# Kernel tuning notes

Measured on AMD Instinct MI355X. Metric: run time of the kernel, lower is better.

Reference implementation:

```python
import jax, jax.numpy as jnp
import numpy as np

N, E, G, H = 50000, 800000, 2048, 128
DIS = 3  # dis_emb is None -> raw frac_diff (3 dims)
EIN = 2 * H + 6 + DIS  # 265


def _lin_init(key, fan_in, fan_out):
    lim = 1.0 / np.sqrt(fan_in)
    return jax.random.uniform(key, (fan_in, fan_out), jnp.float32, -lim, lim)


def setup_inputs() -> dict:
    key = jax.random.key(0)
    ks = jax.random.split(key, 12)
    node_features = jax.random.normal(ks[0], (N, H), jnp.float32)
    frac_coords = jax.random.uniform(ks[1], (N, 3), jnp.float32)
    lattices = jax.random.normal(ks[2], (G, 6), jnp.float32)
    frac_diff = jax.random.normal(ks[3], (E, 3), jnp.float32)
    edge_index = jax.random.randint(ks[4], (2, E), 0, N, jnp.int64 if jax.config.jax_enable_x64 else jnp.int32)
    edge2graph = jax.random.randint(ks[5], (E,), 0, G, edge_index.dtype)
    return dict(
        node_features=node_features,
        frac_coords=frac_coords,
        lattices=lattices,
        frac_diff=frac_diff,
        edge_index=edge_index,
        edge2graph=edge2graph,
        e_w1=_lin_init(ks[6], EIN, H), e_b1=jnp.zeros((H,), jnp.float32),
        e_w2=_lin_init(ks[7], H, H), e_b2=jnp.zeros((H,), jnp.float32),
        n_w1=_lin_init(ks[8], 2 * H, H), n_b1=jnp.zeros((H,), jnp.float32),
        n_w2=_lin_init(ks[9], H, H), n_b2=jnp.zeros((H,), jnp.float32),
    )


def reference(node_features, frac_coords, lattices, frac_diff, edge_index, edge2graph,
              e_w1, e_b1, e_w2, e_b2, n_w1, n_b1, n_w2, n_b2):
    n_nodes = node_features.shape[0]
    silu = jax.nn.silu
    # edge model: gather endpoints, concat with per-graph lattice + frac_diff
    hi = node_features[edge_index[0]]            # [E, H]
    hj = node_features[edge_index[1]]            # [E, H]
    lat = lattices[edge2graph]                   # [E, 6]
    edges_input = jnp.concatenate([hi, hj, lat, frac_diff], axis=1)  # [E, 265]
    e = silu(edges_input @ e_w1 + e_b1)
    edge_features = silu(e @ e_w2 + e_b2)        # [E, H]
    # scatter-mean aggregate onto source nodes
    seg = edge_index[0]
    agg_sum = jax.ops.segment_sum(edge_features, seg, num_segments=n_nodes)
    cnt = jax.ops.segment_sum(jnp.ones((edge_features.shape[0],), edge_features.dtype), seg, num_segments=n_nodes)
    agg = agg_sum / jnp.maximum(cnt, 1.0)[:, None]
    # node model + residual
    h = jnp.concatenate([node_features, agg], axis=1)  # [N, 2H]
    h = silu(h @ n_w1 + n_b1)
    node_output = silu(h @ n_w2 + n_b2)
    return node_features + node_output
```

## Files before the change

### kernel.cpp

```cpp
#include <hip/hip_runtime.h>

#define N_NODES 50000
#define N_EDGES 800000
#define HDIM 128
#define N_GRAPH 2048

typedef __bf16 bf16x8 __attribute__((ext_vector_type(8)));
typedef float f32x4 __attribute__((ext_vector_type(4)));
typedef float f32x16 __attribute__((ext_vector_type(16)));

static __device__ __forceinline__ unsigned short f2bf(float f) {
    unsigned int u = __float_as_uint(f);
    u += 0x7fffu + ((u >> 16) & 1u);
    return (unsigned short)(u >> 16);
}
static __device__ __forceinline__ float bflo(unsigned int u) { return __uint_as_float(u << 16); }
static __device__ __forceinline__ float bfhi(unsigned int u) { return __uint_as_float(u & 0xFFFF0000u); }

static __device__ __forceinline__ unsigned int cvt_pk_bf16(float lo, float hi) {
    unsigned int r;
    asm("v_cvt_pk_bf16_f32 %0, %1, %2" : "=v"(r) : "v"(lo), "v"(hi));
    return r;
}

static __device__ __forceinline__ float silu_f(float x) {
    float e = __builtin_amdgcn_exp2f(x * -1.44269504f);
    return x * __builtin_amdgcn_rcpf(1.0f + e);
}

#define PREP_BLOCKS 1408
#define HIST_BLOCKS 3125
#define ZERO_BLOCKS 6250
__global__ void prep_hist_kernel(const float* __restrict__ ew1, const float* __restrict__ ew2,
                                 const float* __restrict__ nw1, const float* __restrict__ nw2,
                                 const float* __restrict__ eb1, const float* __restrict__ lattices,
                                 const int* __restrict__ eidx,
                                 unsigned short* __restrict__ W1aT, unsigned short* __restrict__ W1bT,
                                 unsigned short* __restrict__ W2t, unsigned short* __restrict__ N1t,
                                 unsigned short* __restrict__ N2t, unsigned short* __restrict__ Lb,
                                 int* __restrict__ buf, float* __restrict__ agg) {
    const int bid = blockIdx.x;
    if (bid >= PREP_BLOCKS + HIST_BLOCKS) {
        const int idx = (bid - PREP_BLOCKS - HIST_BLOCKS) * 256 + threadIdx.x;
        ((float4*)agg)[idx] = make_float4(0.f, 0.f, 0.f, 0.f);
        return;
    }
    if (bid >= PREP_BLOCKS) {
        int e = (bid - PREP_BLOCKS) * 256 + threadIdx.x;
        if (e < N_EDGES) atomicAdd(&buf[eidx[e]], 1);
        return;
    }
    int i = bid * 256 + threadIdx.x;
    if (i < 16384) {
        int n = i >> 7, k = i & 127;
        W1aT[i] = f2bf(ew1[k * 128 + n]);
    } else if (i < 32768) {
        int j = i - 16384; int n = j >> 7, k = j & 127;
        W1bT[j] = f2bf(ew1[(128 + k) * 128 + n]);
    } else if (i < 49152) {
        int j = i - 32768; int n = j >> 7, k = j & 127;
        W2t[j] = f2bf(ew2[k * 128 + n]);
    } else if (i < 81920) {
        int j = i - 49152; int n = j >> 8, k = j & 255;
        N1t[j] = f2bf(nw1[k * 128 + n]);
    } else if (i < 98304) {
        int j = i - 81920; int n = j >> 7, k = j & 127;
        N2t[j] = f2bf(nw2[k * 128 + n]);
    } else if (i < 98304 + 262144) {
        int j = i - 98304; int g = j >> 7, c = j & 127;
        float s = eb1[c];
#pragma unroll
        for (int t = 0; t < 6; ++t) s += lattices[g * 6 + t] * ew1[(256 + t) * 128 + c];
        Lb[j] = f2bf(s);
    }
}

__global__ __launch_bounds__(1024) void scan_kernel(int* __restrict__ buf) {
    constexpr int CH = 12288;
    __shared__ int lds[CH];
    __shared__ int part[1024];
    __shared__ int carry_s;
    const int t = threadIdx.x;
    if (t == 0) carry_s = 0;
    __syncthreads();
#pragma unroll 1
    for (int base = 0; base < N_NODES; base += CH) {
#pragma unroll
        for (int k = 0; k < CH / 1024; ++k) {
            int f = k * 1024 + t;
            lds[f] = (base + f < N_NODES) ? buf[base + f] : 0;
        }
        __syncthreads();
        int loc[12];
        int s = 0;
#pragma unroll
        for (int i = 0; i < 12; ++i) { loc[i] = lds[t * 12 + i]; s += loc[i]; }
        part[t] = s;
        __syncthreads();
        for (int off = 1; off < 1024; off <<= 1) {
            int tmp = (t >= off) ? part[t - off] : 0;
            __syncthreads();
            part[t] += tmp;
            __syncthreads();
        }
        const int total = part[1023];
        int run = carry_s + part[t] - s;
#pragma unroll
        for (int i = 0; i < 12; ++i) { int tmp = loc[i]; lds[t * 12 + i] = run; run += tmp; }
        __syncthreads();
#pragma unroll
        for (int k = 0; k < CH / 1024; ++k) {
            int f = k * 1024 + t;
            if (base + f < N_NODES) buf[base + f] = lds[f];
        }
        __syncthreads();
        if (t == 0) carry_s += total;
        __syncthreads();
    }
}

#define PERM_BLOCKS2 3125
#define PQ_BLOCKS ((N_NODES + 63) / 64)
__global__ __launch_bounds__(256, 4) void perm_pq_kernel(
    const int* __restrict__ eidx, const int* __restrict__ e2g,
    const float* __restrict__ frac_diff, int* __restrict__ buf,
    unsigned short* __restrict__ perm_lo, unsigned char* __restrict__ perm_hi,
    uint4* __restrict__ rec, const int packed,
    const float* __restrict__ nf, const unsigned short* __restrict__ W1aT,
    const unsigned short* __restrict__ W1bT,
    unsigned short* __restrict__ P, unsigned short* __restrict__ Qm) {
    constexpr int SA = 136;
    __shared__ unsigned short sm[64 * SA];
    const int bid = blockIdx.x;
    const int tid = threadIdx.x;

    if (bid < PERM_BLOCKS2) {
        int e = bid * 256 + tid;
        if (e < N_EDGES) {
            int s = eidx[e];
            int pos = atomicAdd(&buf[s], 1);
            if (packed) {
                int d = eidx[N_EDGES + e];
                int g = e2g[e];
                unsigned int w0 = (unsigned int)s | ((unsigned int)d << 16);
                unsigned int w1 = (unsigned int)g | ((unsigned int)f2bf(frac_diff[3 * e]) << 16);
                unsigned int w2 = (unsigned int)f2bf(frac_diff[3 * e + 1]) |
                                  ((unsigned int)f2bf(frac_diff[3 * e + 2]) << 16);
                rec[pos] = make_uint4(w0, w1, w2, 0u);
            } else {
                perm_lo[pos] = (unsigned short)(e & 0xFFFF);
                perm_hi[pos] = (unsigned char)(e >> 16);
            }
        }
        return;
    }

    const int n0 = (bid - PERM_BLOCKS2) * 64;
    const int mrow = tid >> 2, q = tid & 3;
    {
        const int node = n0 + mrow;
        unsigned short* row = sm + mrow * SA + q * 32;
        if (node < N_NODES) {
            const float4* a4 = (const float4*)(nf + (size_t)node * HDIM) + q * 8;
#pragma unroll
            for (int j = 0; j < 8; ++j) {
                float4 v = a4[j];
                *(ushort4*)(row + 4 * j) = make_ushort4(f2bf(v.x), f2bf(v.y), f2bf(v.z), f2bf(v.w));
            }
        } else {
#pragma unroll
            for (int j = 0; j < 8; ++j) *(ushort4*)(row + 4 * j) = make_ushort4(0, 0, 0, 0);
        }
    }
    __syncthreads();

    const int wave = tid >> 6, lane = tid & 63;
    const int lr = lane & 15, kq = lane >> 4;
    f32x4 acca[8] = {}, accb[8] = {};
    const int arow = (wave * 16 + lr) * SA;
#pragma unroll
    for (int ks = 0; ks < 128; ks += 32) {
        bf16x8 a = *(const bf16x8*)(sm + arow + ks + kq * 8);
#pragma unroll
        for (int nt = 0; nt < 8; ++nt) {
            bf16x8 ba = *(const bf16x8*)(W1aT + (nt * 16 + lr) * 128 + ks + kq * 8);
            acca[nt] = __builtin_amdgcn_mfma_f32_16x16x32_bf16(a, ba, acca[nt], 0, 0, 0);
            bf16x8 bb = *(const bf16x8*)(W1bT + (nt * 16 + lr) * 128 + ks + kq * 8);
            accb[nt] = __builtin_amdgcn_mfma_f32_16x16x32_bf16(a, bb, accb[nt], 0, 0, 0);
        }
    }
    __syncthreads();

    const int node = n0 + mrow;
#pragma unroll
    for (int nt = 0; nt < 8; ++nt) {
        const int col = nt * 16 + lr;
#pragma unroll
        for (int r = 0; r < 4; ++r)
            sm[(wave * 16 + kq * 4 + r) * SA + col] = f2bf(acca[nt][r]);
    }
    __syncthreads();
    if (node < N_NODES) {
        uint4* dst = (uint4*)(P + (size_t)node * HDIM + q * 32);
        const uint4* srcp = (const uint4*)(sm + mrow * SA + q * 32);
#pragma unroll
        for (int j = 0; j < 4; ++j) dst[j] = srcp[j];
    }
    __syncthreads();
#pragma unroll
    for (int nt = 0; nt < 8; ++nt) {
        const int col = nt * 16 + lr;
#pragma unroll
        for (int r = 0; r < 4; ++r)
            sm[(wave * 16 + kq * 4 + r) * SA + col] = f2bf(accb[nt][r]);
    }
    __syncthreads();
    if (node < N_NODES) {
        uint4* dst = (uint4*)(Qm + (size_t)node * HDIM + q * 32);
        const uint4* srcp = (const uint4*)(sm + mrow * SA + q * 32);
#pragma unroll
        for (int j = 0; j < 4; ++j) dst[j] = srcp[j];
    }
}


static __device__ __forceinline__ void build_afrag(
    const uint4* pu, const uint4* qu, const uint4* lu,
    float f0, float f1, float f2,
    const unsigned int* wlds, int hi, bf16x8* afrag) {
#pragma unroll
    for (int kk = 0; kk < 8; ++kk) {
        const unsigned int* wl = wlds + (kk * 2 + hi) * 12;
        const uint4 w0v = *(const uint4*)(wl);
        const uint4 w1v = *(const uint4*)(wl + 4);
        const uint4 w2v = *(const uint4*)(wl + 8);
        const unsigned int* pw = (const unsigned int*)&pu[kk];
        const unsigned int* qw = (const unsigned int*)&qu[kk];
        const unsigned int* lw = (const unsigned int*)&lu[kk];
        const unsigned int* w0w = (const unsigned int*)&w0v;
        const unsigned int* w1w = (const unsigned int*)&w1v;
        const unsigned int* w2w = (const unsigned int*)&w2v;
        unsigned int ow[4];
#pragma unroll
        for (int w = 0; w < 4; ++w) {
            float x0 = bflo(pw[w]) + bflo(qw[w]) + bflo(lw[w])
                     + f0 * bflo(w0w[w]) + f1 * bflo(w1w[w]) + f2 * bflo(w2w[w]);
            float x1 = bfhi(pw[w]) + bfhi(qw[w]) + bfhi(lw[w])
                     + f0 * bfhi(w0w[w]) + f1 * bfhi(w1w[w]) + f2 * bfhi(w2w[w]);
            ow[w] = cvt_pk_bf16(silu_f(x0), silu_f(x1));
        }
        afrag[kk] = *(bf16x8*)ow;
    }
}

static __device__ __forceinline__ void do_mfma(
    const bf16x8* afrag, const unsigned short* __restrict__ W2t,
    int row, int hi, f32x16* acc) {
#pragma unroll
    for (int kk = 0; kk < 8; ++kk) {
#pragma unroll
        for (int t4 = 0; t4 < 4; ++t4) {
            bf16x8 bb = *(const bf16x8*)(W2t + (t4 * 32 + row) * 128 + kk * 16 + hi * 8);
            acc[t4] = __builtin_amdgcn_mfma_f32_32x32x16_bf16(afrag[kk], bb, acc[t4], 0, 0, 0);
        }
    }
}

static __device__ __forceinline__ void epilogue(
    const f32x16* acc, const int* sc, const int* snq,
    int row, int hi, const float* __restrict__ b2, float* __restrict__ agg) {
#pragma unroll
    for (int t4 = 0; t4 < 4; ++t4) {
        const int col = t4 * 32 + row;
        const float bias = b2[col];
        float p[16], tq[4], to[4];
#pragma unroll
        for (int rq = 0; rq < 4; ++rq) {
            float s0 = silu_f(acc[t4][4 * rq + 0] + bias);
            float s1 = silu_f(acc[t4][4 * rq + 1] + bias);
            float s2 = silu_f(acc[t4][4 * rq + 2] + bias);
            float s3 = silu_f(acc[t4][4 * rq + 3] + bias);
            p[4 * rq + 0] = s0;
            p[4 * rq + 1] = s0 + s1;
            p[4 * rq + 2] = p[4 * rq + 1] + s2;
            p[4 * rq + 3] = p[4 * rq + 2] + s3;
            tq[rq] = p[4 * rq + 3];
            to[rq] = __shfl_xor(tq[rq], 32);
        }
        float cum = 0.f;
#pragma unroll
        for (int rq = 0; rq < 4; ++rq) {
            const float off = cum + (hi ? to[rq] : 0.f);
            cum += tq[rq] + to[rq];
#pragma unroll
            for (int i = 0; i < 4; ++i) {
                const int r = 4 * rq + i;
                const float val = p[r] + off;
                const int myrow = 4 * (2 * rq + hi) + i;
                const bool lastg = (myrow == 31);
                const int nxt = (i < 3) ? sc[r + 1] : snq[rq];
                const bool bnd = lastg || (sc[r] != nxt);
                if (bnd) {
                    atomicAdd(&agg[(size_t)sc[r] * HDIM + col], val);
                    if (!lastg) atomicAdd(&agg[(size_t)nxt * HDIM + col], -val);
                }
            }
        }
    }
}

#define EDGE_NWG (N_EDGES / 256)
template <bool PACKED>
static __device__ __forceinline__ void fetch_meta(
    int i, const uint4* __restrict__ rec, const int* __restrict__ eidx,
    const int* __restrict__ e2g, const float* __restrict__ frac_diff,
    const unsigned short* __restrict__ perm_lo, const unsigned char* __restrict__ perm_hi,
    int& src, int& dst, int& g, float& f0, float& f1, float& f2) {
    if (PACKED) {
        const uint4 rv = rec[i];
        src = rv.x & 0xFFFF;
        dst = rv.x >> 16;
        g = rv.y & 0xFFFF;
        f0 = bfhi(rv.y);
        f1 = bflo(rv.z);
        f2 = bfhi(rv.z);
    } else {
        const int e = (int)perm_lo[i] | ((int)perm_hi[i] << 16);
        src = eidx[e];
        dst = eidx[N_EDGES + e];
        g = e2g[e];
        f0 = frac_diff[3 * e];
        f1 = frac_diff[3 * e + 1];
        f2 = frac_diff[3 * e + 2];
    }
}

template <bool PACKED>
__global__ __launch_bounds__(256, 2) void edge_kernel(
    const unsigned short* __restrict__ P, const unsigned short* __restrict__ Qm,
    const unsigned short* __restrict__ Lb, const float* __restrict__ frac_diff,
    const int* __restrict__ eidx, const int* __restrict__ e2g,
    const unsigned short* __restrict__ perm_lo, const unsigned char* __restrict__ perm_hi,
    const uint4* __restrict__ rec,
    const float* __restrict__ e_w1, const unsigned short* __restrict__ W2t,
    const float* __restrict__ b2, float* __restrict__ agg) {
    __shared__ __align__(16) unsigned int wlds[192];
    const int tid = threadIdx.x;
    {
        const float* wrbase = e_w1 + 262 * HDIM;
        if (tid < 192) {
            const int w = tid & 3, rw = (tid >> 2) % 3, hi = (tid / 12) & 1, kk = tid / 24;
            const int c = kk * 16 + hi * 8 + 2 * w;
            wlds[((kk * 2 + hi) * 3 + rw) * 4 + w] =
                (unsigned int)f2bf(wrbase[rw * HDIM + c]) |
                ((unsigned int)f2bf(wrbase[rw * HDIM + c + 1]) << 16);
        }
    }
    __syncthreads();

    const int wv = tid >> 6, lane = tid & 63;
    const int row = lane & 31, hi = lane >> 5;
    const int base = blockIdx.x * 256 + wv * 64;

    int srcA, dstA, gA; float fA0, fA1, fA2;
    fetch_meta<PACKED>(base + row, rec, eidx, e2g, frac_diff, perm_lo, perm_hi,
                       srcA, dstA, gA, fA0, fA1, fA2);
    int srcB, dstB, gB; float fB0, fB1, fB2;
    fetch_meta<PACKED>(base + 32 + row, rec, eidx, e2g, frac_diff, perm_lo, perm_hi,
                       srcB, dstB, gB, fB0, fB1, fB2);

    uint4 puA[8], quA[8], luA[8];
    {
        const size_t pr = (size_t)srcA * HDIM, qr = (size_t)dstA * HDIM, lr = (size_t)gA * HDIM;
#pragma unroll
        for (int kk = 0; kk < 8; ++kk) {
            const int c0 = kk * 16 + hi * 8;
            puA[kk] = *(const uint4*)(P + pr + c0);
            quA[kk] = *(const uint4*)(Qm + qr + c0);
            luA[kk] = *(const uint4*)(Lb + lr + c0);
        }
    }
    uint4 puB[8], quB[8], luB[8];
    {
        const size_t pr = (size_t)srcB * HDIM, qr = (size_t)dstB * HDIM, lr = (size_t)gB * HDIM;
#pragma unroll
        for (int kk = 0; kk < 8; ++kk) {
            const int c0 = kk * 16 + hi * 8;
            puB[kk] = *(const uint4*)(P + pr + c0);
            quB[kk] = *(const uint4*)(Qm + qr + c0);
            luB[kk] = *(const uint4*)(Lb + lr + c0);
        }
    }

    bf16x8 afragA[8];
    build_afrag(puA, quA, luA, fA0, fA1, fA2, wlds, hi, afragA);
    int scA[16], snqA[4];
#pragma unroll
    for (int r = 0; r < 16; ++r) scA[r] = __shfl(srcA, (r & 3) + 8 * (r >> 2) + 4 * hi);
#pragma unroll
    for (int j = 0; j < 4; ++j) snqA[j] = __shfl(srcA, (4 * (2 * j + hi) + 4) & 31);
    f32x16 accA[4] = {};
    do_mfma(afragA, W2t, row, hi, accA);
    epilogue(accA, scA, snqA, row, hi, b2, agg);

    bf16x8 afragB[8];
    build_afrag(puB, quB, luB, fB0, fB1, fB2, wlds, hi, afragB);
    int scB[16], snqB[4];
#pragma unroll
    for (int r = 0; r < 16; ++r) scB[r] = __shfl(srcB, (r & 3) + 8 * (r >> 2) + 4 * hi);
#pragma unroll
    for (int j = 0; j < 4; ++j) snqB[j] = __shfl(srcB, (4 * (2 * j + hi) + 4) & 31);
    f32x16 accB[4] = {};
    do_mfma(afragB, W2t, row, hi, accB);
    epilogue(accB, scB, snqB, row, hi, b2, agg);
}

__global__ __launch_bounds__(256, 4) void node_kernel(
    const float* __restrict__ nf, const float* __restrict__ agg,
    const int* __restrict__ buf,
    const unsigned short* __restrict__ N1t, const float* __restrict__ b1,
    const unsigned short* __restrict__ N2t, const float* __restrict__ b2,
    float* __restrict__ out) {
    constexpr int SA = 264;
    constexpr int S2 = 136;
    constexpr int SFo = 132;
    __shared__ unsigned short sm[64 * SA];
    float* smf = (float*)sm;

    const int tid = threadIdx.x;
    const int n0 = blockIdx.x * 64;
    const int mrow = tid >> 2, q = tid & 3;
    {
        const int node = n0 + mrow;
        unsigned short* row = sm + mrow * SA;
        const int cbq = q * 32;
        if (node < N_NODES) {
            const int c = buf[node] - (node ? buf[node - 1] : 0);
            const float inv = 1.0f / (float)max(c, 1);
            const float4* a4 = (const float4*)(nf + (size_t)node * HDIM) + q * 8;
            const float4* g4 = (const float4*)(agg + (size_t)node * HDIM) + q * 8;
#pragma unroll
            for (int j = 0; j < 8; ++j) {
                float4 v = a4[j];
                *(ushort4*)(row + cbq + 4 * j) =
                    make_ushort4(f2bf(v.x), f2bf(v.y), f2bf(v.z), f2bf(v.w));
                float4 g = g4[j];
                *(ushort4*)(row + HDIM + cbq + 4 * j) =
                    make_ushort4(f2bf(g.x * inv), f2bf(g.y * inv), f2bf(g.z * inv), f2bf(g.w * inv));
            }
        } else {
#pragma unroll
            for (int j = 0; j < 8; ++j) {
                *(ushort4*)(row + cbq + 4 * j) = make_ushort4(0, 0, 0, 0);
                *(ushort4*)(row + HDIM + cbq + 4 * j) = make_ushort4(0, 0, 0, 0);
            }
        }
    }
    __syncthreads();

    const int wave = tid >> 6, lane = tid & 63;
    const int lr = lane & 15, kq = lane >> 4;

    f32x4 acc[8] = {};
    const int arow = (wave * 16 + lr) * SA;
#pragma unroll
    for (int ks = 0; ks < 256; ks += 32) {
        bf16x8 a = *(const bf16x8*)(sm + arow + ks + kq * 8);
#pragma unroll
        for (int nt = 0; nt < 8; ++nt) {
            bf16x8 bb = *(const bf16x8*)(N1t + (nt * 16 + lr) * 256 + ks + kq * 8);
            acc[nt] = __builtin_amdgcn_mfma_f32_16x16x32_bf16(a, bb, acc[nt], 0, 0, 0);
        }
    }
    __syncthreads();

#pragma unroll
    for (int nt = 0; nt < 8; ++nt) {
        const int col = nt * 16 + lr;
        const float bias = b1[col];
#pragma unroll
        for (int r = 0; r < 4; ++r) {
            const int mm = wave * 16 + kq * 4 + r;
            sm[mm * S2 + col] = f2bf(silu_f(acc[nt][r] + bias));
        }
    }
    __syncthreads();

    f32x4 acc2[8] = {};
    const int arow2 = (wave * 16 + lr) * S2;
#pragma unroll
    for (int ks = 0; ks < 128; ks += 32) {
        bf16x8 a = *(const bf16x8*)(sm + arow2 + ks + kq * 8);
#pragma unroll
        for (int nt = 0; nt < 8; ++nt) {
            bf16x8 bb = *(const bf16x8*)(N2t + (nt * 16 + lr) * 128 + ks + kq * 8);
            acc2[nt] = __builtin_amdgcn_mfma_f32_16x16x32_bf16(a, bb, acc2[nt], 0, 0, 0);
        }
    }
    __syncthreads();

#pragma unroll
    for (int nt = 0; nt < 8; ++nt) {
        const int col = nt * 16 + lr;
        const float bias = b2[col];
#pragma unroll
        for (int r = 0; r < 4; ++r) {
            const int mm = wave * 16 + kq * 4 + r;
            smf[mm * SFo + col] = silu_f(acc2[nt][r] + bias);
        }
    }
    __syncthreads();
    {
        const int node = n0 + mrow;
        if (node < N_NODES) {
            const float4* nfr = (const float4*)(nf + (size_t)node * HDIM) + q * 8;
            float4* outr = (float4*)(out + (size_t)node * HDIM) + q * 8;
            const float* st = smf + mrow * SFo + q * 32;
#pragma unroll
            for (int j = 0; j < 8; ++j) {
                float4 v = nfr[j];
                float4 s4 = *(const float4*)(st + 4 * j);
                v.x += s4.x; v.y += s4.y; v.z += s4.z; v.w += s4.w;
                outr[j] = v;
            }
        }
    }
}

extern "C" void kernel_launch(void* const* d_in, const int* in_sizes, int n_in,
                              void* d_out, int out_size, void* d_ws, size_t ws_size,
                              hipStream_t stream) {
    const float* node_features = (const float*)d_in[0];
    const float* lattices = (const float*)d_in[2];
    const float* frac_diff = (const float*)d_in[3];
    const int* edge_index = (const int*)d_in[4];
    const int* edge2graph = (const int*)d_in[5];
    const float* e_w1 = (const float*)d_in[6];
    const float* e_b1 = (const float*)d_in[7];
    const float* e_w2 = (const float*)d_in[8];
    const float* e_b2 = (const float*)d_in[9];
    const float* n_w1 = (const float*)d_in[10];
    const float* n_b1 = (const float*)d_in[11];
    const float* n_w2 = (const float*)d_in[12];
    const float* n_b2 = (const float*)d_in[13];

    char* ws = (char*)d_ws;
    unsigned short* W1aT = (unsigned short*)(ws);
    unsigned short* W1bT = (unsigned short*)(ws + 32768);
    unsigned short* W2t  = (unsigned short*)(ws + 65536);
    unsigned short* N1t  = (unsigned short*)(ws + 98304);
    unsigned short* N2t  = (unsigned short*)(ws + 163840);
    unsigned short* Lb   = (unsigned short*)(ws + 196608);
    unsigned short* P    = (unsigned short*)(ws + 720896);
    unsigned short* Qm   = (unsigned short*)(ws + 13520896);
    int* buf             = (int*)(ws + 26320896);
    unsigned short* perm_lo = (unsigned short*)(ws + 26520896);
    unsigned char* perm_hi  = (unsigned char*)(ws + 28120896);
    uint4* rec           = (uint4*)(ws + 28920896);
    float* agg = (float*)d_out;

    const int packed = (ws_size >= 28920896 + (size_t)N_EDGES * 16) ? 1 : 0;

    hipMemsetAsync(buf, 0, (size_t)N_NODES * 4, stream);

    prep_hist_kernel<<<PREP_BLOCKS + HIST_BLOCKS + ZERO_BLOCKS, 256, 0, stream>>>(
        e_w1, e_w2, n_w1, n_w2, e_b1, lattices, edge_index,
        W1aT, W1bT, W2t, N1t, N2t, Lb, buf, agg);

    scan_kernel<<<1, 1024, 0, stream>>>(buf);

    perm_pq_kernel<<<PERM_BLOCKS2 + PQ_BLOCKS, 256, 0, stream>>>(
        edge_index, edge2graph, frac_diff, buf, perm_lo, perm_hi, rec, packed,
        node_features, W1aT, W1bT, P, Qm);

    if (packed) {
        edge_kernel<true><<<EDGE_NWG, 256, 0, stream>>>(
            P, Qm, Lb, frac_diff, edge_index, edge2graph, perm_lo, perm_hi, rec,
            e_w1, W2t, e_b2, agg);
    } else {
        edge_kernel<false><<<EDGE_NWG, 256, 0, stream>>>(
            P, Qm, Lb, frac_diff, edge_index, edge2graph, perm_lo, perm_hi, rec,
            e_w1, W2t, e_b2, agg);
    }

    node_kernel<<<(N_NODES + 63) / 64, 256, 0, stream>>>(
        node_features, agg, buf, N1t, n_b1, N2t, n_b2, (float*)d_out);
}
```

Before: 515.1 us.

## Software-pipeline four edge tiles per wave, wave-shuffle scan, raise MFMA priority

The edge kernel now runs 128-thread blocks where each wave processes four 32-edge tiles instead of two. The gather for the next tile is issued before the current tile's compute, so memory latency overlaps with MFMA and epilogue work. The scan kernel replaces its 1024-step LDS Hillis-Steele loop, with its many barriers, by wave-level shuffle scans plus a serial 16-entry combine. s_setprio is raised around the MFMA loop. Holding more prefetched tiles increases register pressure and may reduce occupancy.

Measured after the change: 638.3 us. +23.9%, slower.

```diff
diff --git a/kernel.cpp b/kernel.cpp
--- a/kernel.cpp
+++ b/kernel.cpp
@@ -78,9 +78,10 @@
 __global__ __launch_bounds__(1024) void scan_kernel(int* __restrict__ buf) {
     constexpr int CH = 12288;
     __shared__ int lds[CH];
-    __shared__ int part[1024];
+    __shared__ int wpart[16];
     __shared__ int carry_s;
     const int t = threadIdx.x;
+    const int wave = t >> 6, lane = t & 63;
     if (t == 0) carry_s = 0;
     __syncthreads();
 #pragma unroll 1
@@ -95,16 +96,22 @@
         int s = 0;
 #pragma unroll
         for (int i = 0; i < 12; ++i) { loc[i] = lds[t * 12 + i]; s += loc[i]; }
-        part[t] = s;
+        int ps = s;
+#pragma unroll
+        for (int off = 1; off < 64; off <<= 1) {
+            int v = __shfl_up(ps, off);
+            if (lane >= off) ps += v;
+        }
+        if (lane == 63) wpart[wave] = ps;
         __syncthreads();
-        for (int off = 1; off < 1024; off <<= 1) {
-            int tmp = (t >= off) ? part[t - off] : 0;
-            __syncthreads();
-            part[t] += tmp;
-            __syncthreads();
-        }
-        const int total = part[1023];
-        int run = carry_s + part[t] - s;
+        if (t == 0) {
+            int r = carry_s;
+#pragma unroll
+            for (int i = 0; i < 16; ++i) { int v = wpart[i]; wpart[i] = r; r += v; }
+            carry_s = r;
+        }
+        __syncthreads();
+        int run = wpart[wave] + (ps - s);
 #pragma unroll
         for (int i = 0; i < 12; ++i) { int tmp = loc[i]; lds[t * 12 + i] = run; run += tmp; }
         __syncthreads();
@@ -113,8 +120,6 @@
             int f = k * 1024 + t;
             if (base + f < N_NODES) buf[base + f] = lds[f];
         }
-        __syncthreads();
-        if (t == 0) carry_s += total;
         __syncthreads();
     }
 }
@@ -256,6 +261,7 @@
 static __device__ __forceinline__ void do_mfma(
     const bf16x8* afrag, const unsigned short* __restrict__ W2t,
     int row, int hi, f32x16* acc) {
+    __builtin_amdgcn_s_setprio(1);
 #pragma unroll
     for (int kk = 0; kk < 8; ++kk) {
 #pragma unroll
@@ -264,6 +270,7 @@
             acc[t4] = __builtin_amdgcn_mfma_f32_32x32x16_bf16(afrag[kk], bb, acc[t4], 0, 0, 0);
         }
     }
+    __builtin_amdgcn_s_setprio(0);
 }
 
 static __device__ __forceinline__ void epilogue(
@@ -335,8 +342,29 @@
     }
 }
 
+static __device__ __forceinline__ void gather_rows(
+    const unsigned short* __restrict__ P, const unsigned short* __restrict__ Qm,
+    const unsigned short* __restrict__ Lb,
+    int src, int dst, int g, int hi, uint4* pu, uint4* qu, uint4* lu) {
+    const size_t pr = (size_t)src * HDIM, qr = (size_t)dst * HDIM, lr = (size_t)g * HDIM;
+#pragma unroll
+    for (int kk = 0; kk < 8; ++kk) {
+        const int c0 = kk * 16 + hi * 8;
+        pu[kk] = *(const uint4*)(P + pr + c0);
+        qu[kk] = *(const uint4*)(Qm + qr + c0);
+        lu[kk] = *(const uint4*)(Lb + lr + c0);
+    }
+}
+
+static __device__ __forceinline__ void make_sc(int src, int hi, int* sc, int* snq) {
+#pragma unroll
+    for (int r = 0; r < 16; ++r) sc[r] = __shfl(src, (r & 3) + 8 * (r >> 2) + 4 * hi);
+#pragma unroll
+    for (int j = 0; j < 4; ++j) snq[j] = __shfl(src, (4 * (2 * j + hi) + 4) & 31);
+}
+
 template <bool PACKED>
-__global__ __launch_bounds__(256, 2) void edge_kernel(
+__global__ __launch_bounds__(128, 2) void edge_kernel(
     const unsigned short* __restrict__ P, const unsigned short* __restrict__ Qm,
     const unsigned short* __restrict__ Lb, const float* __restrict__ frac_diff,
     const int* __restrict__ eidx, const int* __restrict__ e2g,
@@ -348,8 +376,8 @@
     const int tid = threadIdx.x;
     {
         const float* wrbase = e_w1 + 262 * HDIM;
-        if (tid < 192) {
-            const int w = tid & 3, rw = (tid >> 2) % 3, hi = (tid / 12) & 1, kk = tid / 24;
+        for (int t = tid; t < 192; t += 128) {
+            const int w = t & 3, rw = (t >> 2) % 3, hi = (t / 12) & 1, kk = t / 24;
             const int c = kk * 16 + hi * 8 + 2 * w;
             wlds[((kk * 2 + hi) * 3 + rw) * 4 + w] =
                 (unsigned int)f2bf(wrbase[rw * HDIM + c]) |
@@ -360,7 +388,7 @@
 
     const int wv = tid >> 6, lane = tid & 63;
     const int row = lane & 31, hi = lane >> 5;
-    const int base = blockIdx.x * 256 + wv * 64;
+    const int base = (blockIdx.x * 2 + wv) * 128;
 
     int srcA, dstA, gA; float fA0, fA1, fA2;
     fetch_meta<PACKED>(base + row, rec, eidx, e2g, frac_diff, perm_lo, perm_hi,
@@ -368,51 +396,55 @@
     int srcB, dstB, gB; float fB0, fB1, fB2;
     fetch_meta<PACKED>(base + 32 + row, rec, eidx, e2g, frac_diff, perm_lo, perm_hi,
                        srcB, dstB, gB, fB0, fB1, fB2);
+    int srcC, dstC, gC; float fC0, fC1, fC2;
+    fetch_meta<PACKED>(base + 64 + row, rec, eidx, e2g, frac_diff, perm_lo, perm_hi,
+                       srcC, dstC, gC, fC0, fC1, fC2);
+    int srcD, dstD, gD; float fD0, fD1, fD2;
+    fetch_meta<PACKED>(base + 96 + row, rec, eidx, e2g, frac_diff, perm_lo, perm_hi,
+                       srcD, dstD, gD, fD0, fD1, fD2);
 
     uint4 puA[8], quA[8], luA[8];
-    {
-        const size_t pr = (size_t)srcA * HDIM, qr = (size_t)dstA * HDIM, lr = (size_t)gA * HDIM;
-#pragma unroll
-        for (int kk = 0; kk < 8; ++kk) {
-            const int c0 = kk * 16 + hi * 8;
-            puA[kk] = *(const uint4*)(P + pr + c0);
-            quA[kk] = *(const uint4*)(Qm + qr + c0);
-            luA[kk] = *(const uint4*)(Lb + lr + c0);
-        }
-    }
+    gather_rows(P, Qm, Lb, srcA, dstA, gA, hi, puA, quA, luA);
     uint4 puB[8], quB[8], luB[8];
-    {
-        const size_t pr = (size_t)srcB * HDIM, qr = (size_t)dstB * HDIM, lr = (size_t)gB * HDIM;
-#pragma unroll
-        for (int kk = 0; kk < 8; ++kk) {
-            const int c0 = kk * 16 + hi * 8;
-            puB[kk] = *(const uint4*)(P + pr + c0);
-            quB[kk] = *(const uint4*)(Qm + qr + c0);
-            luB[kk] = *(const uint4*)(Lb + lr + c0);
-        }
-    }
+    gather_rows(P, Qm, Lb, srcB, dstB, gB, hi, puB, quB, luB);
 
     bf16x8 afragA[8];
     build_afrag(puA, quA, luA, fA0, fA1, fA2, wlds, hi, afragA);
     int scA[16], snqA[4];
-#pragma unroll
-    for (int r = 0; r < 16; ++r) scA[r] = __shfl(srcA, (r & 3) + 8 * (r >> 2) + 4 * hi);
-#pragma unroll
-    for (int j = 0; j < 4; ++j) snqA[j] = __shfl(srcA, (4 * (2 * j + hi) + 4) & 31);
+    make_sc(srcA, hi, scA, snqA);
     f32x16 accA[4] = {};
     do_mfma(afragA, W2t, row, hi, accA);
     epilogue(accA, scA, snqA, row, hi, b2, agg);
 
+    uint4 puC[8], quC[8], luC[8];
+    gather_rows(P, Qm, Lb, srcC, dstC, gC, hi, puC, quC, luC);
+
     bf16x8 afragB[8];
     build_afrag(puB, quB, luB, fB0, fB1, fB2, wlds, hi, afragB);
     int scB[16], snqB[4];
-#pragma unroll
-    for (int r = 0; r < 16; ++r) scB[r] = __shfl(srcB, (r & 3) + 8 * (r >> 2) + 4 * hi);
-#pragma unroll
-    for (int j = 0; j < 4; ++j) snqB[j] = __shfl(srcB, (4 * (2 * j + hi) + 4) & 31);
+    make_sc(srcB, hi, scB, snqB);
     f32x16 accB[4] = {};
     do_mfma(afragB, W2t, row, hi, accB);
     epilogue(accB, scB, snqB, row, hi, b2, agg);
+
+    uint4 puD[8], quD[8], luD[8];
+    gather_rows(P, Qm, Lb, srcD, dstD, gD, hi, puD, quD, luD);
+
+    bf16x8 afragC[8];
+    build_afrag(puC, quC, luC, fC0, fC1, fC2, wlds, hi, afragC);
+    int scC[16], snqC[4];
+    make_sc(srcC, hi, scC, snqC);
+    f32x16 accC[4] = {};
+    do_mfma(afragC, W2t, row, hi, accC);
+    epilogue(accC, scC, snqC, row, hi, b2, agg);
+
+    bf16x8 afragD[8];
+    build_afrag(puD, quD, luD, fD0, fD1, fD2, wlds, hi, afragD);
+    int scD[16], snqD[4];
+    make_sc(srcD, hi, scD, snqD);
+    f32x16 accD[4] = {};
+    do_mfma(afragD, W2t, row, hi, accD);
+    epilogue(accD, scD, snqD, row, hi, b2, agg);
 }
 
 __global__ __launch_bounds__(256, 4) void node_kernel(
@@ -574,11 +606,11 @@
         node_features, W1aT, W1bT, P, Qm);
 
     if (packed) {
-        edge_kernel<true><<<EDGE_NWG, 256, 0, stream>>>(
+        edge_kernel<true><<<EDGE_NWG, 128, 0, stream>>>(
             P, Qm, Lb, frac_diff, edge_index, edge2graph, perm_lo, perm_hi, rec,
             e_w1, W2t, e_b2, agg);
     } else {
-        edge_kernel<false><<<EDGE_NWG, 256, 0, stream>>>(
+        edge_kernel<false><<<EDGE_NWG, 128, 0, stream>>>(
             P, Qm, Lb, frac_diff, edge_index, edge2graph, perm_lo, perm_hi, rec,
             e_w1, W2t, e_b2, agg);
     }
```
